# Kernel optimization log

Measured on AMD Instinct MI355X. Metric: run time of the kernel, lower is better.

Reference implementation:

```python
import jax, jax.numpy as jnp
import numpy as np


def setup_inputs() -> dict:
    key = jax.random.key(0)
    k0, k1, k2, k3, k4 = jax.random.split(key, 5)
    feat0 = jax.random.normal(k0, (32, 256, 56, 56), dtype=jnp.float32)
    feat1 = jax.random.normal(k1, (32, 512, 28, 28), dtype=jnp.float32)
    feat2 = jax.random.normal(k2, (32, 1024, 14, 14), dtype=jnp.float32)
    feat3 = jax.random.normal(k3, (32, 2048, 7, 7), dtype=jnp.float32)
    # Conv2d(3840 -> 1024, kernel_size=1, bias=False): weight [emb, C_total]
    conv_w = jax.random.normal(k4, (1024, 3840), dtype=jnp.float32) * 0.02
    return {"feat0": feat0, "feat1": feat1, "feat2": feat2, "feat3": feat3, "conv_w": conv_w}


def reference(feat0, feat1, feat2, feat3, conv_w):
    # Target spatial size = earliest (largest) level.
    Ht, Wt = feat0.shape[2], feat0.shape[3]

    def up_mean(f):
        # Bilinear upsample (torch Upsample align_corners=False == jax 'bilinear'
        # half-pixel resize), then spatial mean per channel.  Because the 1x1
        # conv and global avg-pool are linear, pooling each upsampled level
        # first and applying the conv on the pooled vector is exactly the
        # same math as conv(concat(upsampled)) followed by avg-pool.
        B, C = f.shape[0], f.shape[1]
        up = jax.image.resize(f, (B, C, Ht, Wt), method='bilinear')  # [B,C,Ht,Wt]
        return jnp.mean(up, axis=(2, 3))  # [B,C]

    v = jnp.concatenate([up_mean(f) for f in (feat0, feat1, feat2, feat3)], axis=1)  # [B, 3840]
    # 1x1 conv (no bias) on pooled vector == GEMM with conv weight, then squeeze.
    return v @ conv_w.T  # [B, emb]
```

## Files before the change

kernel.cpp:

```cpp
#include <hip/hip_runtime.h>


#define NPLANES0 8192
#define NPLANES1 16384
#define NPLANES2 32768
#define NPLANES3 65536
#define TOTAL_PLANES 122880

__global__ __launch_bounds__(256) void pool_kernel(
    const float* __restrict__ f0, const float* __restrict__ f1,
    const float* __restrict__ f2, const float* __restrict__ f3,
    float* __restrict__ v)
{
    int wid  = (blockIdx.x << 2) + (threadIdx.x >> 6);
    int lane = threadIdx.x & 63;
    float s = 0.f;
    int b, col;
    float inv;
    if (wid < NPLANES0) {
        int q = wid;
        const float4* p = (const float4*)(f0 + (size_t)q * 3136);
        #pragma unroll
        for (int t = 0; t < 12; ++t) {
            float4 x = p[lane + (t << 6)];
            s += x.x + x.y + x.z + x.w;
        }
        if (lane < 16) { float4 x = p[768 + lane]; s += x.x + x.y + x.z + x.w; }
        b = q >> 8; col = q & 255; inv = 1.f / 3136.f;
    } else if (wid < NPLANES0 + NPLANES1) {
        int q = wid - NPLANES0;
        const float4* p = (const float4*)(f1 + (size_t)q * 784);
        #pragma unroll
        for (int t = 0; t < 3; ++t) {
            float4 x = p[lane + (t << 6)];
            s += x.x + x.y + x.z + x.w;
        }
        if (lane < 4) { float4 x = p[192 + lane]; s += x.x + x.y + x.z + x.w; }
        b = q >> 9; col = 256 + (q & 511); inv = 1.f / 784.f;
    } else if (wid < NPLANES0 + NPLANES1 + NPLANES2) {
        int q = wid - (NPLANES0 + NPLANES1);
        const float4* p = (const float4*)(f2 + (size_t)q * 196);
        if (lane < 49) { float4 x = p[lane]; s += x.x + x.y + x.z + x.w; }
        b = q >> 10; col = 768 + (q & 1023); inv = 1.f / 196.f;
    } else {
        int q = wid - (NPLANES0 + NPLANES1 + NPLANES2);
        const float* p = f3 + (size_t)q * 49;
        if (lane < 49) s = p[lane];
        b = q >> 11; col = 1792 + (q & 2047); inv = 1.f / 49.f;
    }
    #pragma unroll
    for (int off = 32; off >= 1; off >>= 1) s += __shfl_xor(s, off);
    if (lane == 0) v[b * 3840 + col] = s * inv;
}

#define KT 120
#define LDP 124

__global__ __launch_bounds__(256) void gemm_kernel(
    const float* __restrict__ v, const float* __restrict__ W,
    float* __restrict__ partials)
{
    __shared__ float vs[32][LDP];
    __shared__ float ws[128][LDP];
    int t  = threadIdx.x;
    int et = blockIdx.x & 7;
    int ks = blockIdx.x >> 3;
    int e0 = et << 7;
    int k0 = ks * KT;

    #pragma unroll
    for (int j = 0; j < 4; ++j) {
        int f = t + (j << 8);
        if (f < 960) {
            int row = f / 30, c4 = f % 30;
            *(float4*)&vs[row][c4 * 4] =
                *(const float4*)&v[row * 3840 + k0 + c4 * 4];
        }
    }
    #pragma unroll
    for (int j = 0; j < 15; ++j) {
        int f = t + (j << 8);
        int row = f / 30, c4 = f % 30;
        *(float4*)&ws[row][c4 * 4] =
            *(const float4*)&W[(size_t)(e0 + row) * 3840 + k0 + c4 * 4];
    }
    __syncthreads();

    int bg = t >> 5, eg = t & 31;
    int b0 = bg << 2;
    float acc[4][4] = {};
    #pragma unroll 6
    for (int k = 0; k < KT; k += 4) {
        float4 vv[4], ww[4];
        #pragma unroll
        for (int i = 0; i < 4; ++i) vv[i] = *(const float4*)&vs[b0 + i][k];
        #pragma unroll
        for (int j = 0; j < 4; ++j) ww[j] = *(const float4*)&ws[eg + (j << 5)][k];
        #pragma unroll
        for (int i = 0; i < 4; ++i)
            #pragma unroll
            for (int j = 0; j < 4; ++j)
                acc[i][j] += vv[i].x * ww[j].x + vv[i].y * ww[j].y +
                             vv[i].z * ww[j].z + vv[i].w * ww[j].w;
    }

    float* pout = partials + (size_t)ks * 32768;
    #pragma unroll
    for (int i = 0; i < 4; ++i)
        #pragma unroll
        for (int j = 0; j < 4; ++j)
            pout[(b0 + i) * 1024 + e0 + eg + (j << 5)] = acc[i][j];
}

__global__ __launch_bounds__(256) void reduce_kernel(
    const float* __restrict__ partials, float* __restrict__ out)
{
    int idx = blockIdx.x * 256 + threadIdx.x;
    float s = 0.f;
    #pragma unroll
    for (int ksp = 0; ksp < 32; ++ksp) s += partials[ksp * 32768 + idx];
    out[idx] = s;
}

extern "C" void kernel_launch(void* const* d_in, const int* in_sizes, int n_in,
                              void* d_out, int out_size, void* d_ws, size_t ws_size,
                              hipStream_t stream)
{
    const float* f0 = (const float*)d_in[0];
    const float* f1 = (const float*)d_in[1];
    const float* f2 = (const float*)d_in[2];
    const float* f3 = (const float*)d_in[3];
    const float* W  = (const float*)d_in[4];
    float* out = (float*)d_out;

    float* v        = (float*)d_ws;
    float* partials = v + 32 * 3840;

    pool_kernel<<<TOTAL_PLANES / 4, 256, 0, stream>>>(f0, f1, f2, f3, v);
    gemm_kernel<<<256, 256, 0, stream>>>(v, W, partials);
    reduce_kernel<<<32768 / 256, 256, 0, stream>>>(partials, out);
}
```

Measured before the change: 240.6 us.

## Pool via contiguous 3136-float block chunks through LDS and split GEMM tiles finer

The pooling kernel now gives each block a contiguous 12.5 KB chunk. For level 0 that chunk is one plane, reduced across four waves. For the smaller levels the chunk is staged in LDS and reduced by sub-groups sized to the plane, so every global load is a fully coalesced float4 instead of partial-wave or scalar loads on tiny planes. The GEMM tile is halved to 64 embeddings per block, doubling the grid to 512 blocks for better occupancy, at the cost of re-reading the pooled vector more often. LDS staging adds syncs and shared memory use per block.

Result: faster. 233.7 us (-2.8%).

```diff
diff --git a/kernel.cpp b/kernel.cpp
--- a/kernel.cpp
+++ b/kernel.cpp
@@ -1,115 +1,157 @@
 #include <hip/hip_runtime.h>
 
-
-#define NPLANES0 8192
-#define NPLANES1 16384
-#define NPLANES2 32768
-#define NPLANES3 65536
-#define TOTAL_PLANES 122880
 
 __global__ __launch_bounds__(256) void pool_kernel(
     const float* __restrict__ f0, const float* __restrict__ f1,
     const float* __restrict__ f2, const float* __restrict__ f3,
     float* __restrict__ v)
 {
-    int wid  = (blockIdx.x << 2) + (threadIdx.x >> 6);
-    int lane = threadIdx.x & 63;
-    float s = 0.f;
-    int b, col;
-    float inv;
-    if (wid < NPLANES0) {
-        int q = wid;
-        const float4* p = (const float4*)(f0 + (size_t)q * 3136);
+    __shared__ float l[3136];
+    int bid = blockIdx.x;
+    int t = threadIdx.x;
+
+    if (bid < 8192) {
+        const float4* p = (const float4*)(f0 + (size_t)bid * 3136);
+        float4 a = p[t], b2 = p[t + 256], c = p[t + 512];
+        float s = a.x + a.y + a.z + a.w
+                + b2.x + b2.y + b2.z + b2.w
+                + c.x + c.y + c.z + c.w;
+        if (t < 16) { float4 d = p[t + 768]; s += d.x + d.y + d.z + d.w; }
         #pragma unroll
-        for (int t = 0; t < 12; ++t) {
-            float4 x = p[lane + (t << 6)];
-            s += x.x + x.y + x.z + x.w;
+        for (int o = 32; o; o >>= 1) s += __shfl_xor(s, o);
+        if ((t & 63) == 0) l[t >> 6] = s;
+        __syncthreads();
+        if (t == 0)
+            v[(bid >> 8) * 3840 + (bid & 255)] =
+                (l[0] + l[1] + l[2] + l[3]) * (1.f / 3136.f);
+        return;
+    }
+
+    float4* lf = (float4*)l;
+    if (bid < 12288) {
+        int blk = bid - 8192;
+        const float4* src = (const float4*)(f1 + (size_t)blk * 3136);
+        lf[t] = src[t]; lf[t + 256] = src[t + 256]; lf[t + 512] = src[t + 512];
+        if (t < 16) lf[t + 768] = src[t + 768];
+        __syncthreads();
+        int w = t >> 6, lane = t & 63;
+        const float* base = l + w * 784;
+        float s = 0.f;
+        #pragma unroll
+        for (int i = 0; i < 12; ++i) s += base[lane + (i << 6)];
+        if (lane < 16) s += base[768 + lane];
+        #pragma unroll
+        for (int o = 32; o; o >>= 1) s += __shfl_xor(s, o);
+        if (lane == 0) {
+            int q = blk * 4 + w;
+            v[(q >> 9) * 3840 + 256 + (q & 511)] = s * (1.f / 784.f);
         }
-        if (lane < 16) { float4 x = p[768 + lane]; s += x.x + x.y + x.z + x.w; }
-        b = q >> 8; col = q & 255; inv = 1.f / 3136.f;
-    } else if (wid < NPLANES0 + NPLANES1) {
-        int q = wid - NPLANES0;
-        const float4* p = (const float4*)(f1 + (size_t)q * 784);
+    } else if (bid < 14336) {
+        int blk = bid - 12288;
+        const float4* src = (const float4*)(f2 + (size_t)blk * 3136);
+        lf[t] = src[t]; lf[t + 256] = src[t + 256]; lf[t + 512] = src[t + 512];
+        if (t < 16) lf[t + 768] = src[t + 768];
+        __syncthreads();
+        int p = t >> 4, j = t & 15;
+        const float* base = l + p * 196;
+        float s = 0.f;
         #pragma unroll
-        for (int t = 0; t < 3; ++t) {
-            float4 x = p[lane + (t << 6)];
-            s += x.x + x.y + x.z + x.w;
+        for (int i = 0; i < 12; ++i) s += base[j + (i << 4)];
+        if (j < 4) s += base[192 + j];
+        s += __shfl_xor(s, 8); s += __shfl_xor(s, 4);
+        s += __shfl_xor(s, 2); s += __shfl_xor(s, 1);
+        if (j == 0) {
+            int q = blk * 16 + p;
+            v[(q >> 10) * 3840 + 768 + (q & 1023)] = s * (1.f / 196.f);
         }
-        if (lane < 4) { float4 x = p[192 + lane]; s += x.x + x.y + x.z + x.w; }
-        b = q >> 9; col = 256 + (q & 511); inv = 1.f / 784.f;
-    } else if (wid < NPLANES0 + NPLANES1 + NPLANES2) {
-        int q = wid - (NPLANES0 + NPLANES1);
-        const float4* p = (const float4*)(f2 + (size_t)q * 196);
-        if (lane < 49) { float4 x = p[lane]; s += x.x + x.y + x.z + x.w; }
-        b = q >> 10; col = 768 + (q & 1023); inv = 1.f / 196.f;
     } else {
-        int q = wid - (NPLANES0 + NPLANES1 + NPLANES2);
-        const float* p = f3 + (size_t)q * 49;
-        if (lane < 49) s = p[lane];
-        b = q >> 11; col = 1792 + (q & 2047); inv = 1.f / 49.f;
+        int blk = bid - 14336;
+        const float4* src = (const float4*)(f3 + (size_t)blk * 3136);
+        lf[t] = src[t]; lf[t + 256] = src[t + 256]; lf[t + 512] = src[t + 512];
+        if (t < 16) lf[t + 768] = src[t + 768];
+        __syncthreads();
+        int p = t >> 2, j = t & 3;
+        const float* base = l + p * 49;
+        float s = 0.f;
+        #pragma unroll
+        for (int i = 0; i < 12; ++i) s += base[j + (i << 2)];
+        if (j == 0) s += base[48];
+        s += __shfl_xor(s, 2); s += __shfl_xor(s, 1);
+        if (j == 0) {
+            int q = blk * 64 + p;
+            v[(q >> 11) * 3840 + 1792 + (q & 2047)] = s * (1.f / 49.f);
+        }
     }
-    #pragma unroll
-    for (int off = 32; off >= 1; off >>= 1) s += __shfl_xor(s, off);
-    if (lane == 0) v[b * 3840 + col] = s * inv;
 }
 
 #define KT 120
-#define LDP 124
 
 __global__ __launch_bounds__(256) void gemm_kernel(
     const float* __restrict__ v, const float* __restrict__ W,
     float* __restrict__ partials)
 {
-    __shared__ float vs[32][LDP];
-    __shared__ float ws[128][LDP];
-    int t  = threadIdx.x;
-    int et = blockIdx.x & 7;
-    int ks = blockIdx.x >> 3;
-    int e0 = et << 7;
-    int k0 = ks * KT;
+    __shared__ float vs[32][124];
+    __shared__ float wsh[64][124];
+    int t = threadIdx.x;
+    int et = blockIdx.x & 15, ks = blockIdx.x >> 4;
+    int e0 = et << 6, k0 = ks * KT;
 
-    #pragma unroll
-    for (int j = 0; j < 4; ++j) {
-        int f = t + (j << 8);
-        if (f < 960) {
+    {
+        int f = t;
+        #pragma unroll
+        for (int i = 0; i < 3; ++i, f += 256) {
+            int row = f / 30, c4 = f % 30;
+            *(float4*)&vs[row][c4 * 4] =
+                *(const float4*)&v[row * 3840 + k0 + c4 * 4];
+        }
+        if (t < 192) {
+            f = t + 768;
             int row = f / 30, c4 = f % 30;
             *(float4*)&vs[row][c4 * 4] =
                 *(const float4*)&v[row * 3840 + k0 + c4 * 4];
         }
     }
-    #pragma unroll
-    for (int j = 0; j < 15; ++j) {
-        int f = t + (j << 8);
-        int row = f / 30, c4 = f % 30;
-        *(float4*)&ws[row][c4 * 4] =
-            *(const float4*)&W[(size_t)(e0 + row) * 3840 + k0 + c4 * 4];
+    {
+        int f = t;
+        #pragma unroll
+        for (int i = 0; i < 7; ++i, f += 256) {
+            int row = f / 30, c4 = f % 30;
+            *(float4*)&wsh[row][c4 * 4] =
+                *(const float4*)&W[(size_t)(e0 + row) * 3840 + k0 + c4 * 4];
+        }
+        if (t < 128) {
+            f = t + 1792;
+            int row = f / 30, c4 = f % 30;
+            *(float4*)&wsh[row][c4 * 4] =
+                *(const float4*)&W[(size_t)(e0 + row) * 3840 + k0 + c4 * 4];
+        }
     }
     __syncthreads();
 
     int bg = t >> 5, eg = t & 31;
     int b0 = bg << 2;
-    float acc[4][4] = {};
-    #pragma unroll 6
+    float acc[4][2] = {};
+    #pragma unroll 5
     for (int k = 0; k < KT; k += 4) {
-        float4 vv[4], ww[4];
+        float4 vv[4], ww[2];
         #pragma unroll
         for (int i = 0; i < 4; ++i) vv[i] = *(const float4*)&vs[b0 + i][k];
         #pragma unroll
-        for (int j = 0; j < 4; ++j) ww[j] = *(const float4*)&ws[eg + (j << 5)][k];
+        for (int j = 0; j < 2; ++j) ww[j] = *(const float4*)&wsh[eg + (j << 5)][k];
         #pragma unroll
         for (int i = 0; i < 4; ++i)
             #pragma unroll
-            for (int j = 0; j < 4; ++j)
+            for (int j = 0; j < 2; ++j)
                 acc[i][j] += vv[i].x * ww[j].x + vv[i].y * ww[j].y +
                              vv[i].z * ww[j].z + vv[i].w * ww[j].w;
     }
 
-    float* pout = partials + (size_t)ks * 32768;
+    float* pout = partials + (size_t)ks * 32768 + (size_t)b0 * 1024 + e0 + eg;
     #pragma unroll
     for (int i = 0; i < 4; ++i)
         #pragma unroll
-        for (int j = 0; j < 4; ++j)
-            pout[(b0 + i) * 1024 + e0 + eg + (j << 5)] = acc[i][j];
+        for (int j = 0; j < 2; ++j)
+            pout[i * 1024 + (j << 5)] = acc[i][j];
 }
 
 __global__ __launch_bounds__(256) void reduce_kernel(
@@ -118,7 +160,7 @@
     int idx = blockIdx.x * 256 + threadIdx.x;
     float s = 0.f;
     #pragma unroll
-    for (int ksp = 0; ksp < 32; ++ksp) s += partials[ksp * 32768 + idx];
+    for (int sp = 0; sp < 32; ++sp) s += partials[sp * 32768 + idx];
     out[idx] = s;
 }
 
@@ -136,7 +178,7 @@
     float* v        = (float*)d_ws;
     float* partials = v + 32 * 3840;
 
-    pool_kernel<<<TOTAL_PLANES / 4, 256, 0, stream>>>(f0, f1, f2, f3, v);
-    gemm_kernel<<<256, 256, 0, stream>>>(v, W, partials);
-    reduce_kernel<<<32768 / 256, 256, 0, stream>>>(partials, out);
+    pool_kernel<<<15360, 256, 0, stream>>>(f0, f1, f2, f3, v);
+    gemm_kernel<<<512, 256, 0, stream>>>(v, W, partials);
+    reduce_kernel<<<128, 256, 0, stream>>>(partials, out);
 }
```
